# Kernel optimization log

Hardware: AMD Instinct MI355X
Metric: run time of the kernel (lower is better)

Reference implementation:

```python
import jax, jax.numpy as jnp
import numpy as np

# Static 4-level feature pyramid (H, W) per level; total tokens = 20197
SHAPES = [(100, 152), (50, 76), (25, 38), (13, 19)]
B, S, E, H, L, P, R = 4, 1024, 256, 8, 4, 20, 4
HD = E // H
OFFSET_SCALE = 4.0


def setup_inputs() -> dict:
    key = jax.random.key(0)
    ks = jax.random.split(key, 11)
    total = sum(h * w for h, w in SHAPES)
    s = 0.02
    return {
        "x": jax.random.normal(ks[0], (B, S, E), jnp.float32),
        "encoder_input": jax.random.normal(ks[1], (B, total, E), jnp.float32),
        "v_w": jax.random.normal(ks[2], (E, E), jnp.float32) * s,
        "out_w": jax.random.normal(ks[3], (E, E), jnp.float32) * s,
        "off_w": jax.random.normal(ks[4], (H * L * P * 2, E), jnp.float32) * s,
        "off_b": jax.random.normal(ks[5], (H * L * P * 2,), jnp.float32) * s,
        "attn_w": jax.random.normal(ks[6], (H * L * P, E), jnp.float32) * s,
        "attn_b": jax.random.normal(ks[7], (H * L * P,), jnp.float32) * s,
        "ref_w": jax.random.normal(ks[8], (H * R, E), jnp.float32) * s,
        "ref_b": jax.random.normal(ks[9], (H * R,), jnp.float32) * s,
        "def_refs": jax.random.uniform(ks[10], (R, 2), jnp.float32, 0.1, 0.9),
        "spatial_shapes": jnp.array(SHAPES, dtype=jnp.int32),
    }


def _grid_sample(img, gx, gy, Hh, Ww):
    """Bilinear grid_sample, padding_mode='zeros', align_corners=False.
    img: (N, C, Hh*Ww); gx, gy: (N, M) in [-1, 1]. Returns (N, C, M)."""
    x = ((gx + 1.0) * Ww - 1.0) * 0.5
    y = ((gy + 1.0) * Hh - 1.0) * 0.5
    x0 = jnp.floor(x)
    y0 = jnp.floor(y)
    wx = x - x0
    wy = y - y0
    x0i = x0.astype(jnp.int32)
    y0i = y0.astype(jnp.int32)
    N, C, _ = img.shape

    def gather(xi, yi):
        valid = (xi >= 0) & (xi < Ww) & (yi >= 0) & (yi < Hh)
        idx = jnp.clip(yi, 0, Hh - 1) * Ww + jnp.clip(xi, 0, Ww - 1)
        v = jnp.take_along_axis(
            img, jnp.broadcast_to(idx[:, None, :], (N, C, idx.shape[-1])), axis=2)
        return v * valid[:, None, :].astype(img.dtype)

    return (gather(x0i, y0i) * ((1 - wx) * (1 - wy))[:, None, :]
            + gather(x0i + 1, y0i) * (wx * (1 - wy))[:, None, :]
            + gather(x0i, y0i + 1) * ((1 - wx) * wy)[:, None, :]
            + gather(x0i + 1, y0i + 1) * (wx * wy)[:, None, :])


def reference(x, encoder_input, v_w, out_w, off_w, off_b, attn_w, attn_b,
              ref_w, ref_b, def_refs, spatial_shapes):
    b, s, _ = x.shape
    values = (encoder_input @ v_w.T).reshape(b, -1, H, HD)
    refs = jax.nn.sigmoid(def_refs)  # (R, 2), default reference points
    ref_mix = jax.nn.softmax((x @ ref_w.T + ref_b).reshape(b, s, H, R), axis=-1)
    anchors = jnp.einsum('bshr,rc->bshc', ref_mix, refs)  # (b, s, H, 2)
    offsets = (x @ off_w.T + off_b).reshape(b, s, H, L, P, 2)
    attn = jax.nn.softmax((x @ attn_w.T + attn_b).reshape(b, s, H, L * P),
                          axis=-1).reshape(b, s, H, L, P)

    out = jnp.zeros((b, s, H, HD), x.dtype)
    start = 0
    for lvl, (hh, ww) in enumerate(SHAPES):  # static per-level loop (L=4)
        img = values[:, start:start + hh * ww]  # (b, hh*ww, H, HD)
        start += hh * ww
        img = img.transpose(0, 2, 3, 1).reshape(b * H, HD, hh * ww)
        norm = jnp.array([max(ww, 1), max(hh, 1)], x.dtype)
        locs = anchors[:, :, :, None, :] + jnp.tanh(offsets[:, :, :, lvl]) * (OFFSET_SCALE / norm)
        grid = jnp.clip(locs, 0.0, 1.0) * 2.0 - 1.0  # (b, s, H, P, 2)
        grid = grid.transpose(0, 2, 1, 3, 4).reshape(b * H, s * P, 2)
        sampled = _grid_sample(img, grid[..., 0], grid[..., 1], hh, ww)  # (b*H, HD, s*P)
        sampled = sampled.reshape(b, H, HD, s, P)
        out = out + jnp.einsum('bhcsp,bshp->bshc', sampled, attn[:, :, :, lvl])
    return out.reshape(b, s, E) @ out_w.T
```

## Files before the change

kernel.cpp:

```cpp
#include <hip/hip_runtime.h>
#include <hip/hip_bf16.h>
#include <math.h>

#define NH 8
#define HD 32
#define EDIM 256
#define NL 4
#define NP 20
#define NR 4
#define SEQ 1024
#define BATCH 4
#define TOTAL 20197
#define OFF_SCALE 4.0f

#define M_ENC (BATCH * TOTAL)
#define KDIM 256
#define LDSW 40

typedef short bf16x8 __attribute__((ext_vector_type(8)));
typedef float f32x4  __attribute__((ext_vector_type(4)));

__device__ __forceinline__ unsigned short f32_to_bf16_rne(float f) {
    unsigned u = __float_as_uint(f);
    return (unsigned short)((u + 0x7fffu + ((u >> 16) & 1u)) >> 16);
}

__global__ __launch_bounds__(256) void cast3_kernel(
    const float* __restrict__ s0, unsigned short* __restrict__ d0, long n0,
    const float* __restrict__ s1, unsigned short* __restrict__ d1, long n1,
    const float* __restrict__ s2, unsigned short* __restrict__ d2, long n2)
{
    long c0 = n0 >> 3, c1 = n1 >> 3, c2 = n2 >> 3;
    long total = c0 + c1 + c2;
    long gid = (long)blockIdx.x * blockDim.x + threadIdx.x;
    long stride = (long)gridDim.x * blockDim.x;
    for (long i = gid; i < total; i += stride) {
        const float* s; unsigned short* d; long e;
        if (i < c0)            { s = s0; d = d0; e = i * 8; }
        else if (i < c0 + c1)  { s = s1; d = d1; e = (i - c0) * 8; }
        else                   { s = s2; d = d2; e = (i - c0 - c1) * 8; }
        float4 a = *reinterpret_cast<const float4*>(s + e);
        float4 b = *reinterpret_cast<const float4*>(s + e + 4);
        float f[8] = {a.x, a.y, a.z, a.w, b.x, b.y, b.z, b.w};
        unsigned short o[8];
        #pragma unroll
        for (int j = 0; j < 8; ++j) o[j] = f32_to_bf16_rne(f[j]);
        *reinterpret_cast<uint4*>(d + e) = *reinterpret_cast<const uint4*>(o);
    }
}

__global__ __launch_bounds__(256) void gemm_bf16a_kernel(
    const unsigned short* __restrict__ A,
    const unsigned short* __restrict__ W,
    const float* __restrict__ bias,
    float* __restrict__ C,
    int M_real, int N)
{
    __shared__ __align__(16) unsigned short As[128 * LDSW];
    __shared__ __align__(16) unsigned short Ws[128 * LDSW];

    const int tid  = threadIdx.x;
    const int m0   = blockIdx.x * 128;
    const int n0   = blockIdx.y * 128;
    const int wave = tid >> 6;
    const int lane = tid & 63;
    const int wr   = wave >> 1;
    const int wc   = wave & 1;
    const int lrow = lane & 15;
    const int kg   = lane >> 4;

    f32x4 acc[4][4] = {};

    for (int k0 = 0; k0 < KDIM; k0 += 32) {
        #pragma unroll
        for (int it = 0; it < 2; ++it) {
            int s   = tid + it * 256;
            int row = s >> 2;
            int ks  = s & 3;
            int gm  = m0 + row;
            uint4 va = make_uint4(0u, 0u, 0u, 0u);
            if (gm < M_real)
                va = *reinterpret_cast<const uint4*>(
                    A + (size_t)gm * KDIM + k0 + ks * 8);
            uint4 vw = *reinterpret_cast<const uint4*>(
                W + (size_t)(n0 + row) * KDIM + k0 + ks * 8);
            *reinterpret_cast<uint4*>(&As[row * LDSW + ks * 8]) = va;
            *reinterpret_cast<uint4*>(&Ws[row * LDSW + ks * 8]) = vw;
        }
        __syncthreads();

        bf16x8 af[4], bfr[4];
        #pragma unroll
        for (int mi = 0; mi < 4; ++mi)
            af[mi] = *reinterpret_cast<const bf16x8*>(
                &As[(wr * 64 + mi * 16 + lrow) * LDSW + kg * 8]);
        #pragma unroll
        for (int nj = 0; nj < 4; ++nj)
            bfr[nj] = *reinterpret_cast<const bf16x8*>(
                &Ws[(wc * 64 + nj * 16 + lrow) * LDSW + kg * 8]);
        #pragma unroll
        for (int mi = 0; mi < 4; ++mi)
            #pragma unroll
            for (int nj = 0; nj < 4; ++nj)
                acc[mi][nj] = __builtin_amdgcn_mfma_f32_16x16x32_bf16(
                    af[mi], bfr[nj], acc[mi][nj], 0, 0, 0);
        __syncthreads();
    }

    #pragma unroll
    for (int mi = 0; mi < 4; ++mi) {
        #pragma unroll
        for (int nj = 0; nj < 4; ++nj) {
            int row_base = m0 + wr * 64 + mi * 16 + kg * 4;
            int col      = n0 + wc * 64 + nj * 16 + lrow;
            float bv = bias ? bias[col] : 0.f;
            #pragma unroll
            for (int r = 0; r < 4; ++r) {
                int row = row_base + r;
                if (row < M_real)
                    C[(size_t)row * N + col] = acc[mi][nj][r] + bv;
            }
        }
    }
}

__global__ __launch_bounds__(256) void gemm_mfma_f32a_kernel(
    const float* __restrict__ A,
    const unsigned short* __restrict__ W,
    const float* __restrict__ bias,
    float* __restrict__ C,
    int M_real, int N)
{
    __shared__ __align__(16) unsigned short As[128 * LDSW];
    __shared__ __align__(16) unsigned short Ws[128 * LDSW];

    const int tid  = threadIdx.x;
    const int m0   = blockIdx.x * 128;
    const int n0   = blockIdx.y * 128;
    const int wave = tid >> 6;
    const int lane = tid & 63;
    const int wr   = wave >> 1;
    const int wc   = wave & 1;
    const int lrow = lane & 15;
    const int kg   = lane >> 4;

    f32x4 acc[4][4] = {};

    for (int k0 = 0; k0 < KDIM; k0 += 32) {
        #pragma unroll
        for (int p = 0; p < 4; ++p) {
            int s   = tid + p * 256;
            int row = s >> 3;
            int sl  = s & 7;
            int gm  = m0 + row;
            float4 v = make_float4(0.f, 0.f, 0.f, 0.f);
            if (gm < M_real)
                v = *reinterpret_cast<const float4*>(&A[(size_t)gm * KDIM + k0 + sl * 4]);
            unsigned short o[4] = {
                f32_to_bf16_rne(v.x), f32_to_bf16_rne(v.y),
                f32_to_bf16_rne(v.z), f32_to_bf16_rne(v.w)};
            *reinterpret_cast<uint2*>(&As[row * LDSW + sl * 4]) =
                *reinterpret_cast<const uint2*>(o);
        }
        #pragma unroll
        for (int it = 0; it < 2; ++it) {
            int s   = tid + it * 256;
            int row = s >> 2;
            int ks  = s & 3;
            uint4 vw = *reinterpret_cast<const uint4*>(
                W + (size_t)(n0 + row) * KDIM + k0 + ks * 8);
            *reinterpret_cast<uint4*>(&Ws[row * LDSW + ks * 8]) = vw;
        }
        __syncthreads();

        bf16x8 af[4], bfr[4];
        #pragma unroll
        for (int mi = 0; mi < 4; ++mi)
            af[mi] = *reinterpret_cast<const bf16x8*>(
                &As[(wr * 64 + mi * 16 + lrow) * LDSW + kg * 8]);
        #pragma unroll
        for (int nj = 0; nj < 4; ++nj)
            bfr[nj] = *reinterpret_cast<const bf16x8*>(
                &Ws[(wc * 64 + nj * 16 + lrow) * LDSW + kg * 8]);
        #pragma unroll
        for (int mi = 0; mi < 4; ++mi)
            #pragma unroll
            for (int nj = 0; nj < 4; ++nj)
                acc[mi][nj] = __builtin_amdgcn_mfma_f32_16x16x32_bf16(
                    af[mi], bfr[nj], acc[mi][nj], 0, 0, 0);
        __syncthreads();
    }

    #pragma unroll
    for (int mi = 0; mi < 4; ++mi) {
        #pragma unroll
        for (int nj = 0; nj < 4; ++nj) {
            int row_base = m0 + wr * 64 + mi * 16 + kg * 4;
            int col      = n0 + wc * 64 + nj * 16 + lrow;
            float bv = bias ? bias[col] : 0.f;
            #pragma unroll
            for (int r = 0; r < 4; ++r) {
                int row = row_base + r;
                if (row < M_real)
                    C[(size_t)row * N + col] = acc[mi][nj][r] + bv;
            }
        }
    }
}

__global__ __launch_bounds__(256) void deform_sample_kernel(
    const float* __restrict__ values,
    const float* __restrict__ x,
    const float* __restrict__ ref_w,
    const float* __restrict__ ref_b,
    const float* __restrict__ proj_off,
    const float* __restrict__ proj_attn,
    const float* __restrict__ def_refs,
    unsigned short* __restrict__ out)
{
    const int row = blockIdx.x;
    const int b   = row >> 10;
    const int tid = threadIdx.x;

    __shared__ float  attn_s[NH * NL * NP];
    __shared__ float  anchors[NH][2];
    __shared__ float  refv[NH * NR];
    __shared__ __align__(16) unsigned int sidx[NH * NL * NP][4];
    __shared__ float4 wcor[NH * NL * NP];

    if (tid >= 96) {
        int i = tid - 96;
        reinterpret_cast<float4*>(attn_s)[i] =
            reinterpret_cast<const float4*>(proj_attn + (size_t)row * 640)[i];
    } else if (tid < 32) {
        float dot = ref_b[tid];
        const float* xr = x + (size_t)row * 256;
        const float* wr = ref_w + (size_t)tid * 256;
        for (int k = 0; k < 256; k += 4) {
            float4 xv = *reinterpret_cast<const float4*>(xr + k);
            float4 wv = *reinterpret_cast<const float4*>(wr + k);
            dot += xv.x * wv.x; dot += xv.y * wv.y;
            dot += xv.z * wv.z; dot += xv.w * wv.w;
        }
        refv[tid] = dot;
    }
    __syncthreads();

    if (tid < NH) {
        const int h = tid;
        float rv[NR];
        float rmax = -1e30f;
        #pragma unroll
        for (int r = 0; r < NR; ++r) {
            rv[r] = refv[h * NR + r];
            rmax = fmaxf(rmax, rv[r]);
        }
        float rsum = 0.f;
        #pragma unroll
        for (int r = 0; r < NR; ++r) { rv[r] = __expf(rv[r] - rmax); rsum += rv[r]; }
        float ax = 0.f, ay = 0.f;
        #pragma unroll
        for (int r = 0; r < NR; ++r) {
            float pr = rv[r] / rsum;
            float sx = 1.f / (1.f + __expf(-def_refs[r * 2 + 0]));
            float sy = 1.f / (1.f + __expf(-def_refs[r * 2 + 1]));
            ax += pr * sx; ay += pr * sy;
        }
        anchors[h][0] = ax; anchors[h][1] = ay;
    }
    {
        const int g = tid >> 5;
        const int l = tid & 31;
        float v0 = attn_s[g * 80 + l];
        float v1 = attn_s[g * 80 + 32 + l];
        float v2 = (l < 16) ? attn_s[g * 80 + 64 + l] : -1e30f;
        float m = fmaxf(fmaxf(v0, v1), v2);
        #pragma unroll
        for (int d = 16; d >= 1; d >>= 1) m = fmaxf(m, __shfl_xor(m, d, 64));
        float e0 = __expf(v0 - m), e1 = __expf(v1 - m);
        float e2 = (l < 16) ? __expf(v2 - m) : 0.f;
        float s = e0 + e1 + e2;
        #pragma unroll
        for (int d = 16; d >= 1; d >>= 1) s += __shfl_xor(s, d, 64);
        float inv = 1.f / s;
        __syncthreads();
        attn_s[g * 80 + l]      = e0 * inv;
        attn_s[g * 80 + 32 + l] = e1 * inv;
        if (l < 16) attn_s[g * 80 + 64 + l] = e2 * inv;
    }
    __syncthreads();

    const int lhh[NL] = {100, 50, 25, 13};
    const int lww[NL] = {152, 76, 38, 19};
    const int lst[NL] = {0, 15200, 19000, 19950};

    for (int e = tid; e < NH * NL * NP; e += 256) {
        int h = e / 80;
        int rem = e - h * 80;
        int l = rem / 20;
        const float2 o = *reinterpret_cast<const float2*>(
            proj_off + (size_t)row * 1280 + e * 2);
        float offx = tanhf(o.x);
        float offy = tanhf(o.y);
        int ww = lww[l], hh = lhh[l];
        float locx = fminf(fmaxf(anchors[h][0] + offx * (OFF_SCALE / (float)ww), 0.f), 1.f);
        float locy = fminf(fmaxf(anchors[h][1] + offy * (OFF_SCALE / (float)hh), 0.f), 1.f);
        float xx = locx * (float)ww - 0.5f;
        float yy = locy * (float)hh - 0.5f;
        float x0f = floorf(xx), y0f = floorf(yy);
        int x0 = (int)x0f, y0 = (int)y0f;
        float wx = xx - x0f, wy = yy - y0f;
        float wa = attn_s[e];

        float bx0 = (x0 >= 0)      ? 1.f : 0.f;
        float bx1 = (x0 < ww - 1)  ? 1.f : 0.f;
        float by0 = (y0 >= 0)      ? 1.f : 0.f;
        float by1 = (y0 < hh - 1)  ? 1.f : 0.f;
        int xc0 = max(x0, 0), xc1 = min(x0 + 1, ww - 1);
        int yc0 = max(y0, 0), yc1 = min(y0 + 1, hh - 1);
        sidx[e][0] = (unsigned int)(lst[l] + yc0 * ww + xc0) << 8;
        sidx[e][1] = (unsigned int)(lst[l] + yc0 * ww + xc1) << 8;
        sidx[e][2] = (unsigned int)(lst[l] + yc1 * ww + xc0) << 8;
        sidx[e][3] = (unsigned int)(lst[l] + yc1 * ww + xc1) << 8;

        float4 w;
        w.x = wa * (1.f - wx) * (1.f - wy) * bx0 * by0;
        w.y = wa * wx * (1.f - wy) * bx1 * by0;
        w.z = wa * (1.f - wx) * wy * bx0 * by1;
        w.w = wa * wx * wy * bx1 * by1;
        wcor[e] = w;
    }
    __syncthreads();

    const int h = tid >> 5;
    const int c = tid & 31;
    const float* vb = values + (size_t)b * TOTAL * 256 + h * 32 + c;
    float acc = 0.f;
    #pragma unroll 4
    for (int i = 0; i < 80; ++i) {
        int e = h * 80 + i;
        uint4 pi = *reinterpret_cast<const uint4*>(&sidx[e][0]);
        float4 w = wcor[e];
        acc += w.x * vb[pi.x];
        acc += w.y * vb[pi.y];
        acc += w.z * vb[pi.z];
        acc += w.w * vb[pi.w];
    }
    out[(size_t)row * 256 + h * 32 + c] = f32_to_bf16_rne(acc);
}

extern "C" void kernel_launch(void* const* d_in, const int* in_sizes, int n_in,
                              void* d_out, int out_size, void* d_ws, size_t ws_size,
                              hipStream_t stream)
{
    const float* x        = (const float*)d_in[0];
    const float* enc      = (const float*)d_in[1];
    const float* v_w      = (const float*)d_in[2];
    const float* out_w    = (const float*)d_in[3];
    const float* off_w    = (const float*)d_in[4];
    const float* off_b    = (const float*)d_in[5];
    const float* attn_w   = (const float*)d_in[6];
    const float* attn_b   = (const float*)d_in[7];
    const float* ref_w    = (const float*)d_in[8];
    const float* ref_b    = (const float*)d_in[9];
    const float* def_refs = (const float*)d_in[10];
    float* out = (float*)d_out;

    const int M_Q    = BATCH * SEQ;
    const int N_OFF  = NH * NL * NP * 2;
    const int N_ATTN = NH * NL * NP;

    float* ws = (float*)d_ws;
    float* values = ws;
    char*  region = (char*)(values + (size_t)M_ENC * EDIM);
    unsigned short* enc_bf16 = (unsigned short*)region;
    float* proj_off  = (float*)region;
    float* proj_attn = proj_off  + (size_t)M_Q * N_OFF;
    unsigned short* attn_out_bf16 = (unsigned short*)(proj_attn + (size_t)M_Q * N_ATTN);
    unsigned short* offw_bf16  = attn_out_bf16 + (size_t)M_Q * EDIM;
    unsigned short* attnw_bf16 = offw_bf16  + (size_t)N_OFF * KDIM;
    unsigned short* outw_bf16  = attnw_bf16 + (size_t)N_ATTN * KDIM;
    unsigned short* vw_bf16 = (unsigned short*)(region + (size_t)M_ENC * KDIM * 2);

    dim3 blk(256);

    cast3_kernel<<<dim3(2048), blk, 0, stream>>>(
        enc, enc_bf16, (long)M_ENC * KDIM,
        v_w, vw_bf16, (long)EDIM * KDIM,
        v_w, vw_bf16, 0L);

    gemm_bf16a_kernel<<<dim3((M_ENC + 127) / 128, EDIM / 128), blk, 0, stream>>>(
        enc_bf16, vw_bf16, nullptr, values, M_ENC, EDIM);

    cast3_kernel<<<dim3(288), blk, 0, stream>>>(
        off_w, offw_bf16, (long)N_OFF * KDIM,
        attn_w, attnw_bf16, (long)N_ATTN * KDIM,
        out_w, outw_bf16, (long)EDIM * KDIM);

    gemm_mfma_f32a_kernel<<<dim3(M_Q / 128, N_OFF / 128), blk, 0, stream>>>(
        x, offw_bf16, off_b, proj_off, M_Q, N_OFF);
    gemm_mfma_f32a_kernel<<<dim3(M_Q / 128, N_ATTN / 128), blk, 0, stream>>>(
        x, attnw_bf16, attn_b, proj_attn, M_Q, N_ATTN);

    deform_sample_kernel<<<dim3(M_Q), blk, 0, stream>>>(
        values, x, ref_w, ref_b, proj_off, proj_attn, def_refs, attn_out_bf16);

    gemm_bf16a_kernel<<<dim3(M_Q / 128, EDIM / 128), blk, 0, stream>>>(
        attn_out_bf16, outw_bf16, nullptr, out, M_Q, EDIM);
}
```

Measured before the change: 329.3 us.

## Fuse encoder cast into value GEMM, store values as bf16, merge query projections

```diff
diff --git a/kernel.cpp b/kernel.cpp
--- a/kernel.cpp
+++ b/kernel.cpp
@@ -16,6 +16,7 @@
 #define M_ENC (BATCH * TOTAL)
 #define KDIM 256
 #define LDSW 40
+#define N_Q 1920
 
 typedef short bf16x8 __attribute__((ext_vector_type(8)));
 typedef float f32x4  __attribute__((ext_vector_type(4)));
@@ -24,21 +25,26 @@
     unsigned u = __float_as_uint(f);
     return (unsigned short)((u + 0x7fffu + ((u >> 16) & 1u)) >> 16);
 }
-
-__global__ __launch_bounds__(256) void cast3_kernel(
+__device__ __forceinline__ float bf16_to_f32(unsigned short u) {
+    return __uint_as_float((unsigned)u << 16);
+}
+
+__global__ __launch_bounds__(256) void cast4_kernel(
     const float* __restrict__ s0, unsigned short* __restrict__ d0, long n0,
     const float* __restrict__ s1, unsigned short* __restrict__ d1, long n1,
-    const float* __restrict__ s2, unsigned short* __restrict__ d2, long n2)
-{
-    long c0 = n0 >> 3, c1 = n1 >> 3, c2 = n2 >> 3;
-    long total = c0 + c1 + c2;
+    const float* __restrict__ s2, unsigned short* __restrict__ d2, long n2,
+    const float* __restrict__ s3, unsigned short* __restrict__ d3, long n3)
+{
+    long c0 = n0 >> 3, c1 = n1 >> 3, c2 = n2 >> 3, c3 = n3 >> 3;
+    long total = c0 + c1 + c2 + c3;
     long gid = (long)blockIdx.x * blockDim.x + threadIdx.x;
     long stride = (long)gridDim.x * blockDim.x;
     for (long i = gid; i < total; i += stride) {
         const float* s; unsigned short* d; long e;
-        if (i < c0)            { s = s0; d = d0; e = i * 8; }
-        else if (i < c0 + c1)  { s = s1; d = d1; e = (i - c0) * 8; }
-        else                   { s = s2; d = d2; e = (i - c0 - c1) * 8; }
+        if (i < c0)                 { s = s0; d = d0; e = i * 8; }
+        else if (i < c0 + c1)       { s = s1; d = d1; e = (i - c0) * 8; }
+        else if (i < c0 + c1 + c2)  { s = s2; d = d2; e = (i - c0 - c1) * 8; }
+        else                        { s = s3; d = d3; e = (i - c0 - c1 - c2) * 8; }
         float4 a = *reinterpret_cast<const float4*>(s + e);
         float4 b = *reinterpret_cast<const float4*>(s + e + 4);
         float f[8] = {a.x, a.y, a.z, a.w, b.x, b.y, b.z, b.w};
@@ -49,10 +55,176 @@
     }
 }
 
+__global__ __launch_bounds__(256) void gemm_f32a_f32out_kernel(
+    const float* __restrict__ A,
+    const unsigned short* __restrict__ W,
+    const float* __restrict__ b0, const float* __restrict__ b1, int bsplit,
+    float* __restrict__ C,
+    int M_real, int N)
+{
+    __shared__ __align__(16) unsigned short As[128 * LDSW];
+    __shared__ __align__(16) unsigned short Ws[128 * LDSW];
+
+    const int tid  = threadIdx.x;
+    const int m0   = blockIdx.x * 128;
+    const int n0   = blockIdx.y * 128;
+    const int wave = tid >> 6;
+    const int lane = tid & 63;
+    const int wr   = wave >> 1;
+    const int wc   = wave & 1;
+    const int lrow = lane & 15;
+    const int kg   = lane >> 4;
+
+    f32x4 acc[4][4] = {};
+
+    for (int k0 = 0; k0 < KDIM; k0 += 32) {
+        #pragma unroll
+        for (int p = 0; p < 4; ++p) {
+            int s   = tid + p * 256;
+            int row = s >> 3;
+            int sl  = s & 7;
+            int gm  = m0 + row;
+            float4 v = make_float4(0.f, 0.f, 0.f, 0.f);
+            if (gm < M_real)
+                v = *reinterpret_cast<const float4*>(&A[(size_t)gm * KDIM + k0 + sl * 4]);
+            unsigned short o[4] = {
+                f32_to_bf16_rne(v.x), f32_to_bf16_rne(v.y),
+                f32_to_bf16_rne(v.z), f32_to_bf16_rne(v.w)};
+            *reinterpret_cast<uint2*>(&As[row * LDSW + sl * 4]) =
+                *reinterpret_cast<const uint2*>(o);
+        }
+        #pragma unroll
+        for (int it = 0; it < 2; ++it) {
+            int s   = tid + it * 256;
+            int row = s >> 2;
+            int ks  = s & 3;
+            uint4 vw = *reinterpret_cast<const uint4*>(
+                W + (size_t)(n0 + row) * KDIM + k0 + ks * 8);
+            *reinterpret_cast<uint4*>(&Ws[row * LDSW + ks * 8]) = vw;
+        }
+        __syncthreads();
+
+        bf16x8 af[4], bfr[4];
+        #pragma unroll
+        for (int mi = 0; mi < 4; ++mi)
+            af[mi] = *reinterpret_cast<const bf16x8*>(
+                &As[(wr * 64 + mi * 16 + lrow) * LDSW + kg * 8]);
+        #pragma unroll
+        for (int nj = 0; nj < 4; ++nj)
+            bfr[nj] = *reinterpret_cast<const bf16x8*>(
+                &Ws[(wc * 64 + nj * 16 + lrow) * LDSW + kg * 8]);
+        #pragma unroll
+        for (int mi = 0; mi < 4; ++mi)
+            #pragma unroll
+            for (int nj = 0; nj < 4; ++nj)
+                acc[mi][nj] = __builtin_amdgcn_mfma_f32_16x16x32_bf16(
+                    af[mi], bfr[nj], acc[mi][nj], 0, 0, 0);
+        __syncthreads();
+    }
+
+    #pragma unroll
+    for (int mi = 0; mi < 4; ++mi) {
+        #pragma unroll
+        for (int nj = 0; nj < 4; ++nj) {
+            int row_base = m0 + wr * 64 + mi * 16 + kg * 4;
+            int col      = n0 + wc * 64 + nj * 16 + lrow;
+            float bv = 0.f;
+            if (b0) bv = (col < bsplit) ? b0[col] : b1[col - bsplit];
+            #pragma unroll
+            for (int r = 0; r < 4; ++r) {
+                int row = row_base + r;
+                if (row < M_real)
+                    C[(size_t)row * N + col] = acc[mi][nj][r] + bv;
+            }
+        }
+    }
+}
+
+__global__ __launch_bounds__(256) void gemm_f32a_bf16out_kernel(
+    const float* __restrict__ A,
+    const unsigned short* __restrict__ W,
+    unsigned short* __restrict__ C,
+    int M_real, int N)
+{
+    __shared__ __align__(16) unsigned short As[128 * LDSW];
+    __shared__ __align__(16) unsigned short Ws[128 * LDSW];
+
+    const int tid  = threadIdx.x;
+    const int m0   = blockIdx.x * 128;
+    const int n0   = blockIdx.y * 128;
+    const int wave = tid >> 6;
+    const int lane = tid & 63;
+    const int wr   = wave >> 1;
+    const int wc   = wave & 1;
+    const int lrow = lane & 15;
+    const int kg   = lane >> 4;
+
+    f32x4 acc[4][4] = {};
+
+    for (int k0 = 0; k0 < KDIM; k0 += 32) {
+        #pragma unroll
+        for (int p = 0; p < 4; ++p) {
+            int s   = tid + p * 256;
+            int row = s >> 3;
+            int sl  = s & 7;
+            int gm  = m0 + row;
+            float4 v = make_float4(0.f, 0.f, 0.f, 0.f);
+            if (gm < M_real)
+                v = *reinterpret_cast<const float4*>(&A[(size_t)gm * KDIM + k0 + sl * 4]);
+            unsigned short o[4] = {
+                f32_to_bf16_rne(v.x), f32_to_bf16_rne(v.y),
+                f32_to_bf16_rne(v.z), f32_to_bf16_rne(v.w)};
+            *reinterpret_cast<uint2*>(&As[row * LDSW + sl * 4]) =
+                *reinterpret_cast<const uint2*>(o);
+        }
+        #pragma unroll
+        for (int it = 0; it < 2; ++it) {
+            int s   = tid + it * 256;
+            int row = s >> 2;
+            int ks  = s & 3;
+            uint4 vw = *reinterpret_cast<const uint4*>(
+                W + (size_t)(n0 + row) * KDIM + k0 + ks * 8);
+            *reinterpret_cast<uint4*>(&Ws[row * LDSW + ks * 8]) = vw;
+        }
+        __syncthreads();
+
+        bf16x8 af[4], bfr[4];
+        #pragma unroll
+        for (int mi = 0; mi < 4; ++mi)
+            af[mi] = *reinterpret_cast<const bf16x8*>(
+                &As[(wr * 64 + mi * 16 + lrow) * LDSW + kg * 8]);
+        #pragma unroll
+        for (int nj = 0; nj < 4; ++nj)
+            bfr[nj] = *reinterpret_cast<const bf16x8*>(
+                &Ws[(wc * 64 + nj * 16 + lrow) * LDSW + kg * 8]);
+        #pragma unroll
+        for (int mi = 0; mi < 4; ++mi)
+            #pragma unroll
+            for (int nj = 0; nj < 4; ++nj)
+                acc[mi][nj] = __builtin_amdgcn_mfma_f32_16x16x32_bf16(
+                    af[mi], bfr[nj], acc[mi][nj], 0, 0, 0);
+        __syncthreads();
+    }
+
+    #pragma unroll
+    for (int mi = 0; mi < 4; ++mi) {
+        #pragma unroll
+        for (int nj = 0; nj < 4; ++nj) {
+            int row_base = m0 + wr * 64 + mi * 16 + kg * 4;
+            int col      = n0 + wc * 64 + nj * 16 + lrow;
+            #pragma unroll
+            for (int r = 0; r < 4; ++r) {
+                int row = row_base + r;
+                if (row < M_real)
+                    C[(size_t)row * N + col] = f32_to_bf16_rne(acc[mi][nj][r]);
+            }
+        }
+    }
+}
+
 __global__ __launch_bounds__(256) void gemm_bf16a_kernel(
     const unsigned short* __restrict__ A,
     const unsigned short* __restrict__ W,
-    const float* __restrict__ bias,
     float* __restrict__ C,
     int M_real, int N)
 {
@@ -113,108 +285,22 @@
         for (int nj = 0; nj < 4; ++nj) {
             int row_base = m0 + wr * 64 + mi * 16 + kg * 4;
             int col      = n0 + wc * 64 + nj * 16 + lrow;
-            float bv = bias ? bias[col] : 0.f;
             #pragma unroll
             for (int r = 0; r < 4; ++r) {
                 int row = row_base + r;
                 if (row < M_real)
-                    C[(size_t)row * N + col] = acc[mi][nj][r] + bv;
+                    C[(size_t)row * N + col] = acc[mi][nj][r];
             }
         }
     }
 }
 
-__global__ __launch_bounds__(256) void gemm_mfma_f32a_kernel(
-    const float* __restrict__ A,
-    const unsigned short* __restrict__ W,
-    const float* __restrict__ bias,
-    float* __restrict__ C,
-    int M_real, int N)
-{
-    __shared__ __align__(16) unsigned short As[128 * LDSW];
-    __shared__ __align__(16) unsigned short Ws[128 * LDSW];
-
-    const int tid  = threadIdx.x;
-    const int m0   = blockIdx.x * 128;
-    const int n0   = blockIdx.y * 128;
-    const int wave = tid >> 6;
-    const int lane = tid & 63;
-    const int wr   = wave >> 1;
-    const int wc   = wave & 1;
-    const int lrow = lane & 15;
-    const int kg   = lane >> 4;
-
-    f32x4 acc[4][4] = {};
-
-    for (int k0 = 0; k0 < KDIM; k0 += 32) {
-        #pragma unroll
-        for (int p = 0; p < 4; ++p) {
-            int s   = tid + p * 256;
-            int row = s >> 3;
-            int sl  = s & 7;
-            int gm  = m0 + row;
-            float4 v = make_float4(0.f, 0.f, 0.f, 0.f);
-            if (gm < M_real)
-                v = *reinterpret_cast<const float4*>(&A[(size_t)gm * KDIM + k0 + sl * 4]);
-            unsigned short o[4] = {
-                f32_to_bf16_rne(v.x), f32_to_bf16_rne(v.y),
-                f32_to_bf16_rne(v.z), f32_to_bf16_rne(v.w)};
-            *reinterpret_cast<uint2*>(&As[row * LDSW + sl * 4]) =
-                *reinterpret_cast<const uint2*>(o);
-        }
-        #pragma unroll
-        for (int it = 0; it < 2; ++it) {
-            int s   = tid + it * 256;
-            int row = s >> 2;
-            int ks  = s & 3;
-            uint4 vw = *reinterpret_cast<const uint4*>(
-                W + (size_t)(n0 + row) * KDIM + k0 + ks * 8);
-            *reinterpret_cast<uint4*>(&Ws[row * LDSW + ks * 8]) = vw;
-        }
-        __syncthreads();
-
-        bf16x8 af[4], bfr[4];
-        #pragma unroll
-        for (int mi = 0; mi < 4; ++mi)
-            af[mi] = *reinterpret_cast<const bf16x8*>(
-                &As[(wr * 64 + mi * 16 + lrow) * LDSW + kg * 8]);
-        #pragma unroll
-        for (int nj = 0; nj < 4; ++nj)
-            bfr[nj] = *reinterpret_cast<const bf16x8*>(
-                &Ws[(wc * 64 + nj * 16 + lrow) * LDSW + kg * 8]);
-        #pragma unroll
-        for (int mi = 0; mi < 4; ++mi)
-            #pragma unroll
-            for (int nj = 0; nj < 4; ++nj)
-                acc[mi][nj] = __builtin_amdgcn_mfma_f32_16x16x32_bf16(
-                    af[mi], bfr[nj], acc[mi][nj], 0, 0, 0);
-        __syncthreads();
-    }
-
-    #pragma unroll
-    for (int mi = 0; mi < 4; ++mi) {
-        #pragma unroll
-        for (int nj = 0; nj < 4; ++nj) {
-            int row_base = m0 + wr * 64 + mi * 16 + kg * 4;
-            int col      = n0 + wc * 64 + nj * 16 + lrow;
-            float bv = bias ? bias[col] : 0.f;
-            #pragma unroll
-            for (int r = 0; r < 4; ++r) {
-                int row = row_base + r;
-                if (row < M_real)
-                    C[(size_t)row * N + col] = acc[mi][nj][r] + bv;
-            }
-        }
-    }
-}
-
 __global__ __launch_bounds__(256) void deform_sample_kernel(
-    const float* __restrict__ values,
+    const unsigned short* __restrict__ values,
     const float* __restrict__ x,
     const float* __restrict__ ref_w,
     const float* __restrict__ ref_b,
-    const float* __restrict__ proj_off,
-    const float* __restrict__ proj_attn,
+    const float* __restrict__ proj_q,
     const float* __restrict__ def_refs,
     unsigned short* __restrict__ out)
 {
@@ -225,24 +311,30 @@
     __shared__ float  attn_s[NH * NL * NP];
     __shared__ float  anchors[NH][2];
     __shared__ float  refv[NH * NR];
-    __shared__ __align__(16) unsigned int sidx[NH * NL * NP][4];
+    __shared__ unsigned int sidx[NH * NL * NP][2];
     __shared__ float4 wcor[NH * NL * NP];
+
+    const float* prow = proj_q + (size_t)row * N_Q;
 
     if (tid >= 96) {
         int i = tid - 96;
         reinterpret_cast<float4*>(attn_s)[i] =
-            reinterpret_cast<const float4*>(proj_attn + (size_t)row * 640)[i];
-    } else if (tid < 32) {
-        float dot = ref_b[tid];
-        const float* xr = x + (size_t)row * 256;
-        const float* wr = ref_w + (size_t)tid * 256;
-        for (int k = 0; k < 256; k += 4) {
+            reinterpret_cast<const float4*>(prow + 1280)[i];
+    } else if (tid < 64) {
+        const int r    = tid >> 1;
+        const int half = tid & 1;
+        const float* xr = x + (size_t)row * 256 + half * 128;
+        const float* wr = ref_w + (size_t)r * 256 + half * 128;
+        float dot = 0.f;
+        #pragma unroll
+        for (int k = 0; k < 128; k += 4) {
             float4 xv = *reinterpret_cast<const float4*>(xr + k);
             float4 wv = *reinterpret_cast<const float4*>(wr + k);
             dot += xv.x * wv.x; dot += xv.y * wv.y;
             dot += xv.z * wv.z; dot += xv.w * wv.w;
         }
-        refv[tid] = dot;
+        dot += __shfl_xor(dot, 1, 64);
+        if (half == 0) refv[r] = dot + ref_b[r];
     }
     __syncthreads();
 
@@ -298,8 +390,7 @@
         int h = e / 80;
         int rem = e - h * 80;
         int l = rem / 20;
-        const float2 o = *reinterpret_cast<const float2*>(
-            proj_off + (size_t)row * 1280 + e * 2);
+        const float2 o = *reinterpret_cast<const float2*>(prow + e * 2);
         float offx = tanhf(o.x);
         float offy = tanhf(o.y);
         int ww = lww[l], hh = lhh[l];
@@ -318,33 +409,38 @@
         float by1 = (y0 < hh - 1)  ? 1.f : 0.f;
         int xc0 = max(x0, 0), xc1 = min(x0 + 1, ww - 1);
         int yc0 = max(y0, 0), yc1 = min(y0 + 1, hh - 1);
-        sidx[e][0] = (unsigned int)(lst[l] + yc0 * ww + xc0) << 8;
-        sidx[e][1] = (unsigned int)(lst[l] + yc0 * ww + xc1) << 8;
-        sidx[e][2] = (unsigned int)(lst[l] + yc1 * ww + xc0) << 8;
-        sidx[e][3] = (unsigned int)(lst[l] + yc1 * ww + xc1) << 8;
+        unsigned int i00 = (unsigned int)(lst[l] + yc0 * ww + xc0);
+        unsigned int i10 = (unsigned int)(lst[l] + yc0 * ww + xc1);
+        unsigned int i01 = (unsigned int)(lst[l] + yc1 * ww + xc0);
+        unsigned int i11 = (unsigned int)(lst[l] + yc1 * ww + xc1);
 
         float4 w;
         w.x = wa * (1.f - wx) * (1.f - wy) * bx0 * by0;
         w.y = wa * wx * (1.f - wy) * bx1 * by0;
         w.z = wa * (1.f - wx) * wy * bx0 * by1;
         w.w = wa * wx * wy * bx1 * by1;
+
+        sidx[e][0] = i00 | (i10 << 16);
+        sidx[e][1] = i01 | (i11 << 16);
         wcor[e] = w;
     }
     __syncthreads();
 
     const int h = tid >> 5;
     const int c = tid & 31;
-    const float* vb = values + (size_t)b * TOTAL * 256 + h * 32 + c;
+    const unsigned short* vb = values + (size_t)b * TOTAL * 256 + h * 32 + c;
     float acc = 0.f;
     #pragma unroll 4
     for (int i = 0; i < 80; ++i) {
         int e = h * 80 + i;
-        uint4 pi = *reinterpret_cast<const uint4*>(&sidx[e][0]);
+        unsigned int p0 = sidx[e][0];
+        unsigned int p1 = sidx[e][1];
         float4 w = wcor[e];
-        acc += w.x * vb[pi.x];
-        acc += w.y * vb[pi.y];
-        acc += w.z * vb[pi.z];
-        acc += w.w * vb[pi.w];
+        float v00 = bf16_to_f32(vb[(size_t)(p0 & 0xffffu) * 256]);
+        float v10 = bf16_to_f32(vb[(size_t)(p0 >> 16) * 256]);
+        float v01 = bf16_to_f32(vb[(size_t)(p1 & 0xffffu) * 256]);
+        float v11 = bf16_to_f32(vb[(size_t)(p1 >> 16) * 256]);
+        acc += w.x * v00 + w.y * v10 + w.z * v01 + w.w * v11;
     }
     out[(size_t)row * 256 + h * 32 + c] = f32_to_bf16_rne(acc);
 }
@@ -370,41 +466,32 @@
     const int N_OFF  = NH * NL * NP * 2;
     const int N_ATTN = NH * NL * NP;
 
-    float* ws = (float*)d_ws;
-    float* values = ws;
-    char*  region = (char*)(values + (size_t)M_ENC * EDIM);
-    unsigned short* enc_bf16 = (unsigned short*)region;
-    float* proj_off  = (float*)region;
-    float* proj_attn = proj_off  + (size_t)M_Q * N_OFF;
-    unsigned short* attn_out_bf16 = (unsigned short*)(proj_attn + (size_t)M_Q * N_ATTN);
+    char* wsb = (char*)d_ws;
+    unsigned short* values_bf16 = (unsigned short*)wsb;
+    float* proj_q = (float*)(wsb + (size_t)M_ENC * KDIM * 2);
+    unsigned short* attn_out_bf16 = (unsigned short*)((char*)proj_q + (size_t)M_Q * N_Q * 4);
     unsigned short* offw_bf16  = attn_out_bf16 + (size_t)M_Q * EDIM;
     unsigned short* attnw_bf16 = offw_bf16  + (size_t)N_OFF * KDIM;
-    unsigned short* outw_bf16  = attnw_bf16 + (size_t)N_ATTN * KDIM;
-    unsigned short* vw_bf16 = (unsigned short*)(region + (size_t)M_ENC * KDIM * 2);
+    unsigned short* vw_bf16    = attnw_bf16 + (size_t)N_ATTN * KDIM;
+    unsigned short* outw_bf16  = vw_bf16    + (size_t)EDIM * KDIM;
 
     dim3 blk(256);
 
-    cast3_kernel<<<dim3(2048), blk, 0, stream>>>(
-        enc, enc_bf16, (long)M_ENC * KDIM,
+    cast4_kernel<<<dim3(304), blk, 0, stream>>>(
         v_w, vw_bf16, (long)EDIM * KDIM,
-        v_w, vw_bf16, 0L);
-
-    gemm_bf16a_kernel<<<dim3((M_ENC + 127) / 128, EDIM / 128), blk, 0, stream>>>(
-        enc_bf16, vw_bf16, nullptr, values, M_ENC, EDIM);
-
-    cast3_kernel<<<dim3(288), blk, 0, stream>>>(
         off_w, offw_bf16, (long)N_OFF * KDIM,
         attn_w, attnw_bf16, (long)N_ATTN * KDIM,
         out_w, outw_bf16, (long)EDIM * KDIM);
 
-    gemm_mfma_f32a_kernel<<<dim3(M_Q / 128, N_OFF / 128), blk, 0, stream>>>(
-        x, offw_bf16, off_b, proj_off, M_Q, N_OFF);
-    gemm_mfma_f32a_kernel<<<dim3(M_Q / 128, N_ATTN / 128), blk, 0, stream>>>(
-        x, attnw_bf16, attn_b, proj_attn, M_Q, N_ATTN);
+    gemm_f32a_bf16out_kernel<<<dim3((M_ENC + 127) / 128, EDIM / 128), blk, 0, stream>>>(
+        enc, vw_bf16, values_bf16, M_ENC, EDIM);
+
+    gemm_f32a_f32out_kernel<<<dim3(M_Q / 128, N_Q / 128), blk, 0, stream>>>(
+        x, offw_bf16, off_b, attn_b, N_OFF, proj_q, M_Q, N_Q);
 
     deform_sample_kernel<<<dim3(M_Q), blk, 0, stream>>>(
-        values, x, ref_w, ref_b, proj_off, proj_attn, def_refs, attn_out_bf16);
+        values_bf16, x, ref_w, ref_b, proj_q, def_refs, attn_out_bf16);
 
     gemm_bf16a_kernel<<<dim3(M_Q / 128, EDIM / 128), blk, 0, stream>>>(
-        attn_out_bf16, outw_bf16, nullptr, out, M_Q, EDIM);
-}
+        attn_out_bf16, outw_bf16, out, M_Q, EDIM);
+}
```

Measured after the change: 292.9 us. -11.1%, faster.
